# Performance work log

Hardware: AMD Instinct MI355X
Metric: run time of the kernel (lower is better)

The kernel has to match this reference:

```python
import jax, jax.numpy as jnp
import numpy as np

N_QUBITS = 14
N_LAYERS = 3
BATCH = 128


def _apply_1q(state, gate, w, n):
    """Apply a single-qubit gate on wire w (PennyLane wire 0 = most significant bit).
    state: (B, 2**n) complex. gate: (2,2) shared or (B,2,2) batched."""
    L, R = 2 ** w, 2 ** (n - 1 - w)
    s = state.reshape(-1, L, 2, R)
    if gate.ndim == 2:
        s = jnp.einsum('ij,aljr->alir', gate, s)
    else:
        s = jnp.einsum('aij,aljr->alir', gate, s)
    return s.reshape(state.shape)


def _apply_cnot(state, c, t, n):
    """CNOT with control wire c, target wire t on (B, 2**n) state."""
    s = state.reshape((-1,) + (2,) * n)
    ca = 1 + c
    s0 = jax.lax.index_in_dim(s, 0, ca, keepdims=False)
    s1 = jax.lax.index_in_dim(s, 1, ca, keepdims=False)
    # axis of target after removing control axis
    ta = 1 + t if t < c else t
    s1 = jnp.flip(s1, axis=ta)
    return jnp.stack([s0, s1], axis=ca).reshape(state.shape)


def _rx_gates(angles):
    """Batched RX gate matrices. angles: (B,) -> (B,2,2) complex64."""
    half = angles * 0.5
    c = jnp.cos(half).astype(jnp.complex64)
    s = (-1j) * jnp.sin(half).astype(jnp.complex64)
    return jnp.stack([jnp.stack([c, s], -1), jnp.stack([s, c], -1)], -2)


def _rot_gate(phi, theta, omega):
    """PennyLane Rot(phi,theta,omega) = RZ(omega) RY(theta) RZ(phi), (2,2) complex."""
    ct = jnp.cos(theta * 0.5).astype(jnp.complex64)
    st = jnp.sin(theta * 0.5).astype(jnp.complex64)
    ep = jnp.exp(-0.5j * (phi + omega))  # e^{-i(phi+omega)/2}
    em = jnp.exp(-0.5j * (phi - omega))  # e^{-i(phi-omega)/2}
    return jnp.stack([
        jnp.stack([ep * ct, -jnp.conj(em) * st]),
        jnp.stack([em * st, jnp.conj(ep) * ct]),
    ]).astype(jnp.complex64)


def _simulate(x, q_weights):
    B, n = x.shape
    state = jnp.zeros((B, 2 ** n), jnp.complex64).at[:, 0].set(1.0)
    # AngleEmbedding: RX(x_i) on wire i
    for w in range(n):
        state = _apply_1q(state, _rx_gates(x[:, w]), w, n)
    # StronglyEntanglingLayers: Rot on each wire, then ring of CNOTs with range r
    n_layers = q_weights.shape[0]
    for l in range(n_layers):
        for w in range(n):
            g = _rot_gate(q_weights[l, w, 0], q_weights[l, w, 1], q_weights[l, w, 2])
            state = _apply_1q(state, g, w, n)
        r = (l % (n - 1)) + 1  # PennyLane default ranges
        for w in range(n):
            state = _apply_cnot(state, w, (w + r) % n, n)
    return state


def _pauli_z_signs(n):
    idx = np.arange(2 ** n, dtype=np.int64)[:, None]
    shifts = np.arange(n - 1, -1, -1, dtype=np.int64)[None, :]  # wire 0 = MSB
    bits = (idx >> shifts) & 1
    return jnp.asarray(1.0 - 2.0 * bits, dtype=jnp.float32)  # (2**n, n)


def setup_inputs() -> dict:
    key = jax.random.key(0)
    k1, k2, k3, k4 = jax.random.split(key, 4)
    x = jax.random.normal(k1, (BATCH, N_QUBITS), dtype=jnp.float32)
    q_weights = jax.random.normal(k2, (N_LAYERS, N_QUBITS, 3), dtype=jnp.float32) * 0.01
    w_lin = jax.random.normal(k3, (1, N_QUBITS), dtype=jnp.float32) / np.sqrt(N_QUBITS)
    b_lin = jax.random.normal(k4, (1,), dtype=jnp.float32) * 0.01
    return {"x": x, "q_weights": q_weights, "w_lin": w_lin, "b_lin": b_lin}


def reference(x, q_weights, w_lin, b_lin):
    n = x.shape[1]
    state = _simulate(x, q_weights)
    probs = (state.real ** 2 + state.imag ** 2).astype(jnp.float32)  # (B, 2**n)
    expvals = probs @ _pauli_z_signs(n)  # (B, n) = <Z_i>
    logits = expvals @ w_lin.T + b_lin  # (B, 1)
    return logits
```

## Files before the change

### kernel.cpp

```cpp
#include <hip/hip_runtime.h>
#include <string.h>

#define NQ 14
#define NSTATE (1 << NQ)
#define NL 3
#define MAXP 12
#define BT 1024
#define NWAVES (BT / 64)
#define NEX 11

struct PassG {
    unsigned cmb8[16];
    unsigned R[10];
    unsigned gidx[4];
    unsigned nw;
    unsigned epm;
    unsigned eg[11];
    unsigned parw[11];
    unsigned pad[2];
};
struct ParamsG {
    PassG pass[MAXP];
    unsigned ms[NQ];
    unsigned fmask[NQ];
    unsigned initIW[10];
};
#define PG_WORDS ((int)(sizeof(ParamsG) / 4))

struct C2x2 { float2 m[2][2]; };

__device__ __forceinline__ float2 cmul(float2 a, float2 b) {
    return make_float2(a.x * b.x - a.y * b.y, a.x * b.y + a.y * b.x);
}
__device__ __forceinline__ float2 cmac(float2 acc, float2 a, float2 b) {
    acc.x = fmaf(a.x, b.x, fmaf(-a.y, b.y, acc.x));
    acc.y = fmaf(a.x, b.y, fmaf(a.y, b.x, acc.y));
    return acc;
}

__device__ __forceinline__ C2x2 rot_gate(const float* qp) {
    float phi = qp[0], th = qp[1], om = qp[2];
    float ct, stt; __sincosf(0.5f * th, &stt, &ct);
    float sa, ca; __sincosf(0.5f * (phi + om), &sa, &ca);
    float sb, cb; __sincosf(0.5f * (phi - om), &sb, &cb);
    C2x2 G;
    G.m[0][0] = make_float2(ca * ct, -sa * ct);
    G.m[0][1] = make_float2(-cb * stt, -sb * stt);
    G.m[1][0] = make_float2(cb * stt, -sb * stt);
    G.m[1][1] = make_float2(ca * ct, sa * ct);
    return G;
}

__device__ __forceinline__ C2x2 fuse_rx(C2x2 G, float ang) {
    float sh, ch; __sincosf(0.5f * ang, &sh, &ch);
    float2 c = make_float2(ch, 0.f), is = make_float2(0.f, -sh);
    C2x2 R;
    #pragma unroll
    for (int i = 0; i < 2; ++i) {
        R.m[i][0] = cmac(cmul(G.m[i][0], c), G.m[i][1], is);
        R.m[i][1] = cmac(cmul(G.m[i][1], c), G.m[i][0], is);
    }
    return R;
}

template<int C>
__device__ __forceinline__ void apply_extra(float2 a[16], const float2* gb,
        unsigned w1, unsigned pw, unsigned rep)
{
    const unsigned sga = w1 & 0x3FFFu;
    const int gi = (int)(w1 >> 16) * 4;
    const unsigned og = __popc(rep & sga) & 1u;
    const unsigned swv = pw ^ (og ? 0xFFFFu : 0u);
    float2 g00 = gb[gi + 0], g01 = gb[gi + 1], g10 = gb[gi + 2], g11 = gb[gi + 3];
    const int LB = C & (-C);
    #pragma unroll
    for (int i = 0; i < 16; ++i) {
        if (!(i & LB)) {
            const int i1 = i ^ C;
            const bool sw = (swv >> i) & 1u;
            float2 x0 = sw ? a[i1] : a[i];
            float2 x1 = sw ? a[i]  : a[i1];
            float2 n0 = cmac(cmul(g00, x0), g01, x1);
            float2 n1 = cmac(cmul(g10, x0), g11, x1);
            a[i]  = sw ? n1 : n0;
            a[i1] = sw ? n0 : n1;
        }
    }
}

#define APPLY_BASIS(PS)                                                     \
    {                                                                       \
        _Pragma("unroll")                                                   \
        for (int q = 0; q < 4; ++q) {                                       \
            if (q < (int)nwr) {                    \
                const int gi = (int)psh.pass[PS].gidx[q] * 4;               \
                float2 g00 = gbuf[gi + 0], g01 = gbuf[gi + 1];              \
                float2 g10 = gbuf[gi + 2], g11 = gbuf[gi + 3];              \
                _Pragma("unroll")                                           \
                for (int i = 0; i < 16; ++i) {                              \
                    if (!((i >> q) & 1)) {                                  \
                        const int i1 = i | (1 << q);                        \
                        float2 a0 = a[i], a1 = a[i1];                       \
                        float2 n0 = cmac(cmul(g00, a0), g01, a1);           \
                        float2 n1 = cmac(cmul(g10, a0), g11, a1);           \
                        a[i] = n0; a[i1] = n1;                              \
                    }                                                       \
                }                                                           \
            }                                                               \
        }                                                                   \
    }

#define APPLY_EXTRAS(PS)                                                    \
    {                                                                       \
        if (epm) {                                                          \
            if (epm & (1u<<0))  apply_extra<3> (a, gbuf, psh.pass[PS].eg[0],  psh.pass[PS].parw[0],  rn); \
            if (epm & (1u<<1))  apply_extra<5> (a, gbuf, psh.pass[PS].eg[1],  psh.pass[PS].parw[1],  rn); \
            if (epm & (1u<<2))  apply_extra<6> (a, gbuf, psh.pass[PS].eg[2],  psh.pass[PS].parw[2],  rn); \
            if (epm & (1u<<3))  apply_extra<9> (a, gbuf, psh.pass[PS].eg[3],  psh.pass[PS].parw[3],  rn); \
            if (epm & (1u<<4))  apply_extra<10>(a, gbuf, psh.pass[PS].eg[4],  psh.pass[PS].parw[4],  rn); \
            if (epm & (1u<<5))  apply_extra<12>(a, gbuf, psh.pass[PS].eg[5],  psh.pass[PS].parw[5],  rn); \
            if (epm & (1u<<6))  apply_extra<7> (a, gbuf, psh.pass[PS].eg[6],  psh.pass[PS].parw[6],  rn); \
            if (epm & (1u<<7))  apply_extra<11>(a, gbuf, psh.pass[PS].eg[7],  psh.pass[PS].parw[7],  rn); \
            if (epm & (1u<<8))  apply_extra<13>(a, gbuf, psh.pass[PS].eg[8],  psh.pass[PS].parw[8],  rn); \
            if (epm & (1u<<9))  apply_extra<14>(a, gbuf, psh.pass[PS].eg[9],  psh.pass[PS].parw[9],  rn); \
            if (epm & (1u<<10)) apply_extra<15>(a, gbuf, psh.pass[PS].eg[10], psh.pass[PS].parw[10], rn); \
        }                                                                   \
    }

__global__ __launch_bounds__(BT, 4) void qsim_kernel(
    const float* __restrict__ x, const float* __restrict__ qw,
    const float* __restrict__ wl, const float* __restrict__ bl,
    float* __restrict__ out, const ParamsG* __restrict__ pp, int np)
{
    __shared__ float2 st[NSTATE];
    __shared__ float2 gbuf[NL * NQ * 4];
    __shared__ float2 ubuf[NQ][2];
    __shared__ float red[NWAVES];
    __shared__ __align__(16) ParamsG psh;

    const int tid = threadIdx.x;
    const int b = blockIdx.x;

    {
        const unsigned* srcw = (const unsigned*)pp;
        unsigned* dstw = (unsigned*)&psh;
        for (int i = tid; i < PG_WORDS; i += BT) dstw[i] = srcw[i];
    }

    if (tid < NL * NQ) {
        int l = tid / NQ, w = tid % NQ;
        C2x2 G = rot_gate(qw + tid * 3);
        if (l == 0) {
            G = fuse_rx(G, x[b * NQ + w]);
            ubuf[w][0] = G.m[0][0];
            ubuf[w][1] = G.m[1][0];
        }
        gbuf[tid * 4 + 0] = G.m[0][0];
        gbuf[tid * 4 + 1] = G.m[0][1];
        gbuf[tid * 4 + 2] = G.m[1][0];
        gbuf[tid * 4 + 3] = G.m[1][1];
    }

    char* sb = (char*)st;
    float2 a[16];
    unsigned addr[16];
    unsigned rn;

    __syncthreads();

    {
        unsigned r0 = 0, b0 = 0;
        #pragma unroll
        for (int j = 0; j < 10; ++j) {
            const unsigned sel = (tid >> j) & 1;
            r0 ^= sel ? psh.pass[0].R[j] : 0u;
            b0 ^= sel ? psh.initIW[j] : 0u;
        }
        rn = r0;
        const unsigned rb = rn << 3;
        float2 c = ubuf[0][b0 & 1];
        #pragma unroll
        for (int w = 1; w < 10; ++w)
            c = cmul(c, ubuf[w][(b0 >> w) & 1]);
        a[0] = cmul(c, ubuf[10][0]);
        a[1] = cmul(c, ubuf[10][1]);
        #pragma unroll
        for (int i = 0; i < 2; ++i) {
            a[2 + i] = cmul(a[i], ubuf[11][1]);
            a[i]     = cmul(a[i], ubuf[11][0]);
        }
        #pragma unroll
        for (int i = 0; i < 4; ++i) {
            a[4 + i] = cmul(a[i], ubuf[12][1]);
            a[i]     = cmul(a[i], ubuf[12][0]);
        }
        #pragma unroll
        for (int i = 0; i < 8; ++i) {
            a[8 + i] = cmul(a[i], ubuf[13][1]);
            a[i]     = cmul(a[i], ubuf[13][0]);
        }
        #pragma unroll
        for (int i = 0; i < 16; ++i)
            *(float2*)(sb + (rb ^ psh.pass[0].cmb8[i])) = a[i];
    }

    {
        unsigned rt = 0;
        #pragma unroll
        for (int j = 0; j < 10; ++j)
            rt ^= ((tid >> j) & 1) ? psh.pass[1].R[j] : 0u;
        rn = rt;
    }

    #pragma unroll 1
    for (int ps = 1; ps < np - 1; ++ps) {
        __syncthreads();
        const unsigned rb = rn << 3;
        #pragma unroll
        for (int i = 0; i < 16; ++i) addr[i] = rb ^ psh.pass[ps].cmb8[i];
        #pragma unroll
        for (int i = 0; i < 16; ++i)
            a[i] = *(const float2*)(sb + addr[i]);
        unsigned rt = 0;
        #pragma unroll
        for (int j = 0; j < 10; ++j)
            rt ^= ((tid >> j) & 1) ? psh.pass[ps + 1].R[j] : 0u;
        const unsigned nwr = psh.pass[ps].nw;
        APPLY_BASIS(ps);
        const unsigned epm = psh.pass[ps].epm;
        APPLY_EXTRAS(ps);
        #pragma unroll
        for (int i = 0; i < 16; ++i)
            *(float2*)(sb + addr[i]) = a[i];
        rn = rt;
    }

    float acc = 0.f;
    {
        const int ps = np - 1;
        __syncthreads();
        const unsigned rb = rn << 3;
        #pragma unroll
        for (int i = 0; i < 16; ++i) addr[i] = rb ^ psh.pass[ps].cmb8[i];
        #pragma unroll
        for (int i = 0; i < 16; ++i)
            a[i] = *(const float2*)(sb + addr[i]);
        const unsigned nwr = psh.pass[ps].nw;
        APPLY_BASIS(ps);
        const unsigned epm = psh.pass[ps].epm;
        APPLY_EXTRAS(ps);

        float A[16];
        #pragma unroll
        for (int i = 0; i < 16; ++i) A[i] = 0.f;
        #pragma unroll
        for (int w = 0; w < NQ; ++w) {
            float v = wl[w];
            unsigned p0 = __popc(rn & psh.ms[w]) & 1u;
            float vs = p0 ? -v : v;
            const unsigned fm = psh.fmask[w];
            #pragma unroll
            for (int i = 0; i < 16; ++i)
                A[i] += ((fm >> i) & 1u) ? -vs : vs;
        }
        #pragma unroll
        for (int i = 0; i < 16; ++i)
            acc = fmaf(fmaf(a[i].x, a[i].x, a[i].y * a[i].y), A[i], acc);
    }

    #pragma unroll
    for (int off = 32; off > 0; off >>= 1) acc += __shfl_down(acc, off, 64);
    if ((tid & 63) == 0) red[tid >> 6] = acc;
    __syncthreads();
    if (tid == 0) {
        float s2 = 0.f;
        #pragma unroll
        for (int i = 0; i < NWAVES; ++i) s2 += red[i];
        out[b] = s2 + bl[0];
    }
}

struct GF2Basis {
    unsigned piv[NQ];
    GF2Basis() { for (int i = 0; i < NQ; ++i) piv[i] = 0; }
    bool insert(unsigned v) {
        for (int bb = NQ - 1; bb >= 0; --bb) {
            if (!((v >> bb) & 1)) continue;
            if (piv[bb]) v ^= piv[bb];
            else { piv[bb] = v; return true; }
        }
        return false;
    }
};

static inline int par16(unsigned v) { return __builtin_parity(v); }
static inline unsigned lcg_next(unsigned& s) { s = s * 1664525u + 1013904223u; return s >> 8; }

static unsigned gf_apply(const unsigned* C, unsigned v) {
    unsigned r = 0;
    while (v) { int j = __builtin_ctz(v); v &= v - 1; r ^= C[j]; }
    return r;
}

static bool gf_invert(const unsigned* C, unsigned* Ci) {
    unsigned rows[NQ], irows[NQ];
    for (int i = 0; i < NQ; ++i) {
        unsigned r = 0;
        for (int j = 0; j < NQ; ++j) r |= ((C[j] >> i) & 1u) << j;
        rows[i] = r; irows[i] = 1u << i;
    }
    for (int c = 0; c < NQ; ++c) {
        int p = -1;
        for (int r = c; r < NQ; ++r) if ((rows[r] >> c) & 1u) { p = r; break; }
        if (p < 0) return false;
        unsigned t = rows[p]; rows[p] = rows[c]; rows[c] = t;
        t = irows[p]; irows[p] = irows[c]; irows[c] = t;
        for (int r = 0; r < NQ; ++r)
            if (r != c && ((rows[r] >> c) & 1u)) { rows[r] ^= rows[c]; irows[r] ^= irows[c]; }
    }
    for (int j = 0; j < NQ; ++j) {
        unsigned col = 0;
        for (int i = 0; i < NQ; ++i) col |= ((irows[i] >> j) & 1u) << i;
        Ci[j] = col;
    }
    return true;
}

extern "C" void kernel_launch(void* const* d_in, const int* in_sizes, int n_in,
                              void* d_out, int out_size, void* d_ws, size_t ws_size,
                              hipStream_t stream) {
    const float* x  = (const float*)d_in[0];
    const float* qw = (const float*)d_in[1];
    const float* wl = (const float*)d_in[2];
    const float* bl = (const float*)d_in[3];
    float* out = (float*)d_out;

    const int B = in_sizes[0] / NQ;

    static const int EXC[NEX] = {3, 5, 6, 9, 10, 12, 7, 11, 13, 14, 15};
    int c2s[16]; for (int i = 0; i < 16; ++i) c2s[i] = -1;
    for (int k = 0; k < NEX; ++k) c2s[EXC[k]] = k;

    unsigned gs[NL * NQ], gm[NL * NQ];
    int ggi[NL * NQ];
    unsigned s[NQ], m[NQ], msIdx[NQ];
    for (int w = 0; w < NQ; ++w) s[w] = m[w] = 1u << (NQ - 1 - w);
    int ng = 0;
    for (int l = 0; l < NL; ++l) {
        if (l > 0) {
            for (int w = 0; w < NQ; ++w) {
                gs[ng] = s[w]; gm[ng] = m[w]; ggi[ng] = l * NQ + w; ++ng;
            }
        }
        int r = (l % (NQ - 1)) + 1;
        for (int w = 0; w < NQ; ++w) {
            int c = w, t = (w + r) % NQ;
            s[t] ^= s[c];
            m[c] ^= m[t];
        }
    }
    for (int w = 0; w < NQ; ++w) msIdx[w] = s[w];

    struct Raw {
        unsigned rv[10], cmb[16];
        unsigned char gidx[4], nw;
        int exgate[NEX];
        unsigned exsel[NEX];
        unsigned exT[NEX];
    } raw[MAXP];
    for (int p = 0; p < MAXP; ++p)
        for (int k = 0; k < NEX; ++k) raw[p].exgate[k] = -1;

    {
        unsigned mm[4];
        for (int q = 0; q < 4; ++q) mm[q] = 1u << (3 - q);
        for (int j = 0; j < 10; ++j) raw[0].rv[j] = 1u << (13 - j);
        for (int idx = 0; idx < 16; ++idx) {
            unsigned c = 0;
            for (int q = 0; q < 4; ++q) if ((idx >> q) & 1) c ^= mm[q];
            raw[0].cmb[idx] = c;
        }
        for (int q = 0; q < 4; ++q) raw[0].gidx[q] = 0;
        raw[0].nw = 0;
    }

    bool used[NL * NQ] = {false};
    int np = 1, remaining = ng;
    while (remaining > 0 && np < MAXP) {
        unsigned pss[4], pmm[4];
        int pgi[4], nw = 0;
        GF2Basis gf;
        for (int g = 0; g < ng && nw < 4; ++g) {
            if (used[g]) continue;
            bool ok = true;
            for (int k = 0; k < nw && ok; ++k)
                if (par16(gs[g] & pmm[k]) || par16(pss[k] & gm[g])) ok = false;
            for (int h = 0; h < g && ok; ++h)
                if (!used[h] && (par16(gs[g] & gm[h]) || par16(gs[h] & gm[g]))) ok = false;
            if (!ok) continue;
            GF2Basis trial = gf;
            if (!trial.insert(gm[g])) continue;
            gf = trial;
            pss[nw] = gs[g]; pmm[nw] = gm[g]; pgi[nw] = g; ++nw;
            used[g] = true; --remaining;
        }
        unsigned mm[4], ss[4];
        for (int i = 0; i < nw; ++i) { mm[i] = pmm[i]; ss[i] = pss[i]; }
        for (int i = nw; i < 4; ++i) {
            unsigned cand = 0;
            for (int t = 0; t < NQ; ++t)
                if (gf.insert(1u << t)) { cand = 1u << t; break; }
            for (int j = 0; j < nw; ++j)
                if (par16(cand & ss[j])) cand ^= mm[j];
            mm[i] = cand; ss[i] = 0;
        }
        int nR = 0;
        for (int t = 0; t < NQ && nR < 10; ++t) {
            if (gf.insert(1u << t)) {
                unsigned v = 1u << t;
                for (int j = 0; j < nw; ++j)
                    if (par16(v & ss[j])) v ^= mm[j];
                raw[np].rv[nR++] = v;
            }
        }
        for (int idx = 0; idx < 16; ++idx) {
            unsigned c = 0;
            for (int q = 0; q < 4; ++q) if ((idx >> q) & 1) c ^= mm[q];
            raw[np].cmb[idx] = c;
        }
        for (int q = 0; q < 4; ++q)
            raw[np].gidx[q] = (unsigned char)(q < nw ? ggi[pgi[q]] : 0);
        raw[np].nw = (unsigned char)nw;

        {
            int exCirc[NEX]; int nExtra = 0;
            for (int g = 0; g < ng; ++g) {
                if (used[g]) continue;
                int c = -1;
                for (int t2 = 3; t2 < 16; ++t2) {
                    if (__builtin_popcount((unsigned)t2) < 2) continue;
                    unsigned xr = 0;
                    for (int j = 0; j < 4; ++j) if ((t2 >> j) & 1) xr ^= mm[j];
                    if (xr == gm[g]) { c = t2; break; }
                }
                if (c < 0) continue;
                int slot = c2s[c];
                if (slot < 0 || raw[np].exgate[slot] >= 0) continue;
                unsigned T = 0;
                for (int j = 0; j < 4; ++j)
                    T |= (unsigned)(par16(mm[j] & gs[g]) & 1) << j;
                {
                    int sp = 0;
                    for (int j = 0; j < 4; ++j) if ((c >> j) & 1) sp ^= (T >> j) & 1;
                    if (!sp) continue;
                }
                bool ok = true;
                for (int e = 0; e < nExtra && ok; ++e) {
                    int h = exCirc[e];
                    if (par16(gs[g] & gm[h]) || par16(gs[h] & gm[g])) ok = false;
                }
                for (int kk = 0; kk < nw && ok; ++kk) {
                    int h = pgi[kk];
                    if (h > g && (par16(gs[g] & gm[h]) || par16(gs[h] & gm[g]))) ok = false;
                }
                for (int h = 0; h < g && ok; ++h)
                    if (!used[h] && (par16(gs[g] & gm[h]) || par16(gs[h] & gm[g]))) ok = false;
                if (!ok) continue;
                raw[np].exgate[slot] = ggi[g];
                raw[np].exsel[slot] = gs[g];
                raw[np].exT[slot] = T;
                exCirc[nExtra++] = g;
                used[g] = true; --remaining;
            }
        }
        ++np;
    }

    unsigned Cm[NQ], Ci[NQ];
    unsigned seed = 0x9E3779B9u;
    bool found = false;
    for (int tries = 0; tries < 5000 && !found; ++tries) {
        for (int j = 0; j < NQ; ++j) Cm[j] = lcg_next(seed) & (NSTATE - 1);
        if (!gf_invert(Cm, Ci)) continue;
        found = true;
        for (int p = 0; p < np && found; ++p) {
            unsigned piv[4] = {0, 0, 0, 0}; int npv = 0;
            for (int i = 0; i < 10; ++i) {
                unsigned w2 = gf_apply(Cm, raw[p].rv[i]);
                for (int bb = 0; bb < 4; ++bb)
                    if (((w2 >> bb) & 1u) && piv[bb]) w2 ^= piv[bb];
                if ((w2 & 15u) && npv < 4) { piv[__builtin_ctz(w2 & 15u)] = w2; ++npv; }
            }
            if (npv < 4) found = false;
        }
    }
    if (!found) {
        for (int j = 0; j < NQ; ++j) Cm[j] = 1u << j;
        gf_invert(Cm, Ci);
    }

    static ParamsG h_pg;
    memset(&h_pg, 0, sizeof(h_pg));
    for (int p = 0; p < np; ++p) {
        unsigned u[10];
        for (int i = 0; i < 10; ++i) u[i] = gf_apply(Cm, raw[p].rv[i]);
        unsigned piv[4] = {0, 0, 0, 0};
        int ord[10], npv = 0, rest[10], nrest = 0;
        for (int i = 0; i < 10; ++i) {
            unsigned w2 = u[i];
            for (int bb = 0; bb < 4; ++bb)
                if (((w2 >> bb) & 1u) && piv[bb]) w2 ^= piv[bb];
            if ((w2 & 15u) && npv < 4) { piv[__builtin_ctz(w2 & 15u)] = w2; ord[npv++] = i; }
            else rest[nrest++] = i;
        }
        int kk = 0;
        for (int i = 0; i < npv; ++i) h_pg.pass[p].R[kk++] = u[ord[i]];
        for (int i = 0; i < nrest; ++i) h_pg.pass[p].R[kk++] = u[rest[i]];
        for (int idx = 0; idx < 16; ++idx)
            h_pg.pass[p].cmb8[idx] = gf_apply(Cm, raw[p].cmb[idx]) << 3;
        for (int q = 0; q < 4; ++q) h_pg.pass[p].gidx[q] = raw[p].gidx[q];
        h_pg.pass[p].nw = raw[p].nw;
        unsigned epm = 0;
        for (int k = 0; k < NEX; ++k) {
            if (raw[p].exgate[k] < 0) continue;
            epm |= 1u << k;
            unsigned sga = 0;
            for (int i = 0; i < NQ; ++i)
                sga |= (unsigned)(par16(Ci[i] & raw[p].exsel[k]) & 1) << i;
            h_pg.pass[p].eg[k] = sga | ((unsigned)raw[p].exgate[k] << 16);
            unsigned T = raw[p].exT[k], pw = 0;
            for (int i = 0; i < 16; ++i)
                pw |= (unsigned)(__builtin_popcount(i & T) & 1) << i;
            h_pg.pass[p].parw[k] = pw;
        }
        h_pg.pass[p].epm = epm;
    }
    for (int w = 0; w < NQ; ++w) {
        unsigned msp = 0;
        for (int i = 0; i < NQ; ++i)
            msp |= (unsigned)(par16(Ci[i] & msIdx[w]) & 1) << i;
        h_pg.ms[w] = msp;
    }
    for (int w = 0; w < NQ; ++w) {
        unsigned fm = 0;
        for (int i = 0; i < 16; ++i)
            fm |= (unsigned)(par16((h_pg.pass[np - 1].cmb8[i] >> 3) & h_pg.ms[w]) & 1) << i;
        h_pg.fmask[w] = fm;
    }
    {
        unsigned tmask[NQ];
        for (int w = 0; w < NQ; ++w) {
            unsigned t = 0;
            for (int i = 0; i < NQ; ++i)
                t |= (unsigned)((Ci[i] >> (NQ - 1 - w)) & 1u) << i;
            tmask[w] = t;
        }
        for (int j = 0; j < 10; ++j) {
            unsigned iw = 0;
            for (int w = 0; w < NQ; ++w)
                iw |= (unsigned)(par16(h_pg.pass[0].R[j] & tmask[w]) & 1) << w;
            h_pg.initIW[j] = iw;
        }
    }

    ParamsG* d_pg = (ParamsG*)d_ws;
    hipMemcpyAsync(d_pg, &h_pg, sizeof(ParamsG), hipMemcpyHostToDevice, stream);
    qsim_kernel<<<dim3(B), dim3(BT), 0, stream>>>(x, qw, wl, bl, out, d_pg, np);
}
```

Measured before the change: 100.6 us.

## Split each batch state across two blocks with a global-memory exchange between halves

Splits the simulation into two kernels, each running two 512-thread blocks per batch element over a half-size (8192-entry) shared state. The circuit's passes are grouped into two halves, each lacking one GF(2) direction, and the state is exchanged through a global workspace buffer between the kernels. This aims to raise parallelism and occupancy, since the old launch used only one large block per element (128 blocks). It adds a global round-trip of the full state, a second launch, and extra host-side planning, with a fallback to the old single kernel when the split is not possible.

```diff
diff --git a/kernel.cpp b/kernel.cpp
--- a/kernel.cpp
+++ b/kernel.cpp
@@ -8,6 +8,66 @@
 #define BT 1024
 #define NWAVES (BT / 64)
 #define NEX 11
+#define BTS 512
+#define NWS (BTS / 64)
+#define HSTATE 8192
+
+
+struct C2x2 { float2 m[2][2]; };
+
+__device__ __forceinline__ float2 cmul(float2 a, float2 b) {
+    return make_float2(a.x * b.x - a.y * b.y, a.x * b.y + a.y * b.x);
+}
+__device__ __forceinline__ float2 cmac(float2 acc, float2 a, float2 b) {
+    acc.x = fmaf(a.x, b.x, fmaf(-a.y, b.y, acc.x));
+    acc.y = fmaf(a.x, b.y, fmaf(a.y, b.x, acc.y));
+    return acc;
+}
+__device__ __forceinline__ C2x2 rot_gate(const float* qp) {
+    float phi = qp[0], th = qp[1], om = qp[2];
+    float ct, stt; __sincosf(0.5f * th, &stt, &ct);
+    float sa, ca; __sincosf(0.5f * (phi + om), &sa, &ca);
+    float sb, cb; __sincosf(0.5f * (phi - om), &sb, &cb);
+    C2x2 G;
+    G.m[0][0] = make_float2(ca * ct, -sa * ct);
+    G.m[0][1] = make_float2(-cb * stt, -sb * stt);
+    G.m[1][0] = make_float2(cb * stt, -sb * stt);
+    G.m[1][1] = make_float2(ca * ct, sa * ct);
+    return G;
+}
+__device__ __forceinline__ C2x2 fuse_rx(C2x2 G, float ang) {
+    float sh, ch; __sincosf(0.5f * ang, &sh, &ch);
+    float2 c = make_float2(ch, 0.f), is = make_float2(0.f, -sh);
+    C2x2 R;
+    #pragma unroll
+    for (int i = 0; i < 2; ++i) {
+        R.m[i][0] = cmac(cmul(G.m[i][0], c), G.m[i][1], is);
+        R.m[i][1] = cmac(cmul(G.m[i][1], c), G.m[i][0], is);
+    }
+    return R;
+}
+
+#define APPLY_BASIS(PS)                                                     \
+    {                                                                       \
+        _Pragma("unroll")                                                   \
+        for (int q = 0; q < 4; ++q) {                                       \
+            if (q < (int)nwr) {                                             \
+                const int gi = (int)psh.pass[PS].gidx[q] * 4;               \
+                float2 g00 = gbuf[gi + 0], g01 = gbuf[gi + 1];              \
+                float2 g10 = gbuf[gi + 2], g11 = gbuf[gi + 3];              \
+                _Pragma("unroll")                                           \
+                for (int i = 0; i < 16; ++i) {                              \
+                    if (!((i >> q) & 1)) {                                  \
+                        const int i1 = i | (1 << q);                        \
+                        float2 a0 = a[i], a1 = a[i1];                       \
+                        float2 n0 = cmac(cmul(g00, a0), g01, a1);           \
+                        float2 n1 = cmac(cmul(g10, a0), g11, a1);           \
+                        a[i] = n0; a[i1] = n1;                              \
+                    }                                                       \
+                }                                                           \
+            }                                                               \
+        }                                                                   \
+    }
 
 struct PassG {
     unsigned cmb8[16];
@@ -26,42 +86,6 @@
     unsigned initIW[10];
 };
 #define PG_WORDS ((int)(sizeof(ParamsG) / 4))
-
-struct C2x2 { float2 m[2][2]; };
-
-__device__ __forceinline__ float2 cmul(float2 a, float2 b) {
-    return make_float2(a.x * b.x - a.y * b.y, a.x * b.y + a.y * b.x);
-}
-__device__ __forceinline__ float2 cmac(float2 acc, float2 a, float2 b) {
-    acc.x = fmaf(a.x, b.x, fmaf(-a.y, b.y, acc.x));
-    acc.y = fmaf(a.x, b.y, fmaf(a.y, b.x, acc.y));
-    return acc;
-}
-
-__device__ __forceinline__ C2x2 rot_gate(const float* qp) {
-    float phi = qp[0], th = qp[1], om = qp[2];
-    float ct, stt; __sincosf(0.5f * th, &stt, &ct);
-    float sa, ca; __sincosf(0.5f * (phi + om), &sa, &ca);
-    float sb, cb; __sincosf(0.5f * (phi - om), &sb, &cb);
-    C2x2 G;
-    G.m[0][0] = make_float2(ca * ct, -sa * ct);
-    G.m[0][1] = make_float2(-cb * stt, -sb * stt);
-    G.m[1][0] = make_float2(cb * stt, -sb * stt);
-    G.m[1][1] = make_float2(ca * ct, sa * ct);
-    return G;
-}
-
-__device__ __forceinline__ C2x2 fuse_rx(C2x2 G, float ang) {
-    float sh, ch; __sincosf(0.5f * ang, &sh, &ch);
-    float2 c = make_float2(ch, 0.f), is = make_float2(0.f, -sh);
-    C2x2 R;
-    #pragma unroll
-    for (int i = 0; i < 2; ++i) {
-        R.m[i][0] = cmac(cmul(G.m[i][0], c), G.m[i][1], is);
-        R.m[i][1] = cmac(cmul(G.m[i][1], c), G.m[i][0], is);
-    }
-    return R;
-}
 
 template<int C>
 __device__ __forceinline__ void apply_extra(float2 a[16], const float2* gb,
@@ -88,28 +112,6 @@
     }
 }
 
-#define APPLY_BASIS(PS)                                                     \
-    {                                                                       \
-        _Pragma("unroll")                                                   \
-        for (int q = 0; q < 4; ++q) {                                       \
-            if (q < (int)nwr) {                    \
-                const int gi = (int)psh.pass[PS].gidx[q] * 4;               \
-                float2 g00 = gbuf[gi + 0], g01 = gbuf[gi + 1];              \
-                float2 g10 = gbuf[gi + 2], g11 = gbuf[gi + 3];              \
-                _Pragma("unroll")                                           \
-                for (int i = 0; i < 16; ++i) {                              \
-                    if (!((i >> q) & 1)) {                                  \
-                        const int i1 = i | (1 << q);                        \
-                        float2 a0 = a[i], a1 = a[i1];                       \
-                        float2 n0 = cmac(cmul(g00, a0), g01, a1);           \
-                        float2 n1 = cmac(cmul(g10, a0), g11, a1);           \
-                        a[i] = n0; a[i1] = n1;                              \
-                    }                                                       \
-                }                                                           \
-            }                                                               \
-        }                                                                   \
-    }
-
 #define APPLY_EXTRAS(PS)                                                    \
     {                                                                       \
         if (epm) {                                                          \
@@ -146,7 +148,6 @@
         unsigned* dstw = (unsigned*)&psh;
         for (int i = tid; i < PG_WORDS; i += BT) dstw[i] = srcw[i];
     }
-
     if (tid < NL * NQ) {
         int l = tid / NQ, w = tid % NQ;
         C2x2 G = rot_gate(qw + tid * 3);
@@ -280,6 +281,312 @@
     }
 }
 
+struct PassK {
+    unsigned cmb8[16];
+    unsigned R[9];
+    unsigned Ug;
+    unsigned gidx[4];
+    unsigned nw, epm;
+    unsigned eg[NEX];
+    unsigned parw[NEX];
+};
+struct ParamsK1 {
+    PassK pass[3];
+    unsigned initIW[9];
+    unsigned initIWg;
+    unsigned SK[12];
+    unsigned SKj, SKg;
+    unsigned pad;
+};
+struct ParamsK2 {
+    PassK pass[3];
+    unsigned SL[13], SLj;
+    unsigned ms[NQ];
+    unsigned fmask[NQ];
+};
+struct ParamsS { ParamsK1 k1; ParamsK2 k2; };
+
+template<int C>
+__device__ __forceinline__ void apply_extra_s(float2 a[16], const float2* gb,
+        unsigned w1, unsigned pw, unsigned rep, unsigned gbit)
+{
+    const int gi = (int)(w1 >> 16) * 4;
+    const unsigned og = ((unsigned)__popc(rep & (w1 & 0x1FFFu)) ^ ((w1 >> 13) & gbit)) & 1u;
+    const unsigned swv = pw ^ (og ? 0xFFFFu : 0u);
+    float2 g00 = gb[gi + 0], g01 = gb[gi + 1], g10 = gb[gi + 2], g11 = gb[gi + 3];
+    const int LB = C & (-C);
+    #pragma unroll
+    for (int i = 0; i < 16; ++i) {
+        if (!(i & LB)) {
+            const int i1 = i ^ C;
+            const bool sw = (swv >> i) & 1u;
+            float2 x0 = sw ? a[i1] : a[i];
+            float2 x1 = sw ? a[i]  : a[i1];
+            float2 n0 = cmac(cmul(g00, x0), g01, x1);
+            float2 n1 = cmac(cmul(g10, x0), g11, x1);
+            a[i]  = sw ? n1 : n0;
+            a[i1] = sw ? n0 : n1;
+        }
+    }
+}
+
+#define APPLY_EXTRAS_S(PS, GB)                                              \
+    {                                                                       \
+        if (epm) {                                                          \
+            if (epm & (1u<<0))  apply_extra_s<3> (a, gbuf, psh.pass[PS].eg[0],  psh.pass[PS].parw[0],  rn, GB); \
+            if (epm & (1u<<1))  apply_extra_s<5> (a, gbuf, psh.pass[PS].eg[1],  psh.pass[PS].parw[1],  rn, GB); \
+            if (epm & (1u<<2))  apply_extra_s<6> (a, gbuf, psh.pass[PS].eg[2],  psh.pass[PS].parw[2],  rn, GB); \
+            if (epm & (1u<<3))  apply_extra_s<9> (a, gbuf, psh.pass[PS].eg[3],  psh.pass[PS].parw[3],  rn, GB); \
+            if (epm & (1u<<4))  apply_extra_s<10>(a, gbuf, psh.pass[PS].eg[4],  psh.pass[PS].parw[4],  rn, GB); \
+            if (epm & (1u<<5))  apply_extra_s<12>(a, gbuf, psh.pass[PS].eg[5],  psh.pass[PS].parw[5],  rn, GB); \
+            if (epm & (1u<<6))  apply_extra_s<7> (a, gbuf, psh.pass[PS].eg[6],  psh.pass[PS].parw[6],  rn, GB); \
+            if (epm & (1u<<7))  apply_extra_s<11>(a, gbuf, psh.pass[PS].eg[7],  psh.pass[PS].parw[7],  rn, GB); \
+            if (epm & (1u<<8))  apply_extra_s<13>(a, gbuf, psh.pass[PS].eg[8],  psh.pass[PS].parw[8],  rn, GB); \
+            if (epm & (1u<<9))  apply_extra_s<14>(a, gbuf, psh.pass[PS].eg[9],  psh.pass[PS].parw[9],  rn, GB); \
+            if (epm & (1u<<10)) apply_extra_s<15>(a, gbuf, psh.pass[PS].eg[10], psh.pass[PS].parw[10], rn, GB); \
+        }                                                                   \
+    }
+
+__global__ __launch_bounds__(BTS, 4) void qsim_k1(
+    const float* __restrict__ x, const float* __restrict__ qw,
+    const ParamsS* __restrict__ pp, float2* __restrict__ stbuf,
+    float* __restrict__ out)
+{
+    __shared__ float2 st[HSTATE];
+    __shared__ float2 gbuf[NL * NQ * 4];
+    __shared__ float2 ubuf[NQ][2];
+    __shared__ ParamsK1 psh;
+
+    const int tid = threadIdx.x;
+    const int e = blockIdx.x >> 1, g1 = blockIdx.x & 1;
+
+    {
+        const unsigned* s = (const unsigned*)&pp->k1;
+        unsigned* d = (unsigned*)&psh;
+        for (int i = tid; i < (int)(sizeof(ParamsK1) / 4); i += BTS) d[i] = s[i];
+    }
+    if (tid < NL * NQ) {
+        int l = tid / NQ, w = tid % NQ;
+        C2x2 G = rot_gate(qw + tid * 3);
+        if (l == 0) {
+            G = fuse_rx(G, x[e * NQ + w]);
+            ubuf[w][0] = G.m[0][0];
+            ubuf[w][1] = G.m[1][0];
+        }
+        gbuf[tid * 4 + 0] = G.m[0][0];
+        gbuf[tid * 4 + 1] = G.m[0][1];
+        gbuf[tid * 4 + 2] = G.m[1][0];
+        gbuf[tid * 4 + 3] = G.m[1][1];
+    }
+    char* sb = (char*)st;
+    __syncthreads();
+
+    {
+        unsigned rn = g1 ? psh.pass[0].Ug : 0u;
+        unsigned b0 = g1 ? psh.initIWg : 0u;
+        #pragma unroll
+        for (int j5 = 0; j5 < 9; ++j5) {
+            const unsigned sel = (tid >> j5) & 1u;
+            rn ^= sel ? psh.pass[0].R[j5] : 0u;
+            b0 ^= sel ? psh.initIW[j5] : 0u;
+        }
+        const unsigned rb = rn << 3;
+        float2 a[16];
+        float2 c = ubuf[0][b0 & 1];
+        #pragma unroll
+        for (int w = 1; w < 10; ++w)
+            c = cmul(c, ubuf[w][(b0 >> w) & 1]);
+        a[0] = cmul(c, ubuf[10][0]);
+        a[1] = cmul(c, ubuf[10][1]);
+        #pragma unroll
+        for (int i = 0; i < 2; ++i) {
+            a[2 + i] = cmul(a[i], ubuf[11][1]);
+            a[i]     = cmul(a[i], ubuf[11][0]);
+        }
+        #pragma unroll
+        for (int i = 0; i < 4; ++i) {
+            a[4 + i] = cmul(a[i], ubuf[12][1]);
+            a[i]     = cmul(a[i], ubuf[12][0]);
+        }
+        #pragma unroll
+        for (int i = 0; i < 8; ++i) {
+            a[8 + i] = cmul(a[i], ubuf[13][1]);
+            a[i]     = cmul(a[i], ubuf[13][0]);
+        }
+        #pragma unroll
+        for (int i = 0; i < 16; ++i)
+            *(float2*)(sb + (rb ^ psh.pass[0].cmb8[i])) = a[i];
+    }
+
+    for (int p5 = 1; p5 < 3; ++p5) {
+        __syncthreads();
+        unsigned rn = g1 ? psh.pass[p5].Ug : 0u;
+        #pragma unroll
+        for (int j5 = 0; j5 < 9; ++j5)
+            rn ^= ((tid >> j5) & 1u) ? psh.pass[p5].R[j5] : 0u;
+        const unsigned rb = rn << 3;
+        unsigned addr[16];
+        #pragma unroll
+        for (int i = 0; i < 16; ++i) addr[i] = rb ^ psh.pass[p5].cmb8[i];
+        float2 a[16];
+        #pragma unroll
+        for (int i = 0; i < 16; ++i) a[i] = *(const float2*)(sb + addr[i]);
+        const unsigned nwr = psh.pass[p5].nw;
+        APPLY_BASIS(p5);
+        const unsigned epm = psh.pass[p5].epm;
+        APPLY_EXTRAS_S(p5, (unsigned)g1);
+        #pragma unroll
+        for (int i = 0; i < 16; ++i) *(float2*)(sb + addr[i]) = a[i];
+    }
+    __syncthreads();
+
+    {
+        unsigned tb = g1 ? psh.SKg : 0u;
+        #pragma unroll
+        for (int k = 0; k < 9; ++k)
+            tb ^= ((tid >> k) & 1u) ? psh.SK[k] : 0u;
+        #pragma unroll
+        for (int j2 = 0; j2 < 2; ++j2) {
+            const unsigned bb = tb ^ (j2 ? psh.SKj : 0u);
+            float2* gdst = stbuf + ((((size_t)e * 2 + j2) * 2 + g1) << 12) + tid;
+            #pragma unroll
+            for (int i = 0; i < 8; ++i) {
+                unsigned la = bb;
+                if (i & 1) la ^= psh.SK[9];
+                if (i & 2) la ^= psh.SK[10];
+                if (i & 4) la ^= psh.SK[11];
+                gdst[i * 512] = *(const float2*)(sb + la);
+            }
+        }
+        if (g1 == 0 && tid == 0) out[e] = 0.f;
+    }
+}
+
+__global__ __launch_bounds__(BTS, 4) void qsim_k2(
+    const float* __restrict__ x, const float* __restrict__ qw,
+    const float* __restrict__ wl, const float* __restrict__ bl,
+    const ParamsS* __restrict__ pp, const float2* __restrict__ stbuf,
+    float* __restrict__ out)
+{
+    __shared__ float2 st[HSTATE];
+    __shared__ float2 gbuf[NL * NQ * 4];
+    __shared__ float2 ubuf[NQ][2];
+    __shared__ ParamsK2 psh;
+    __shared__ float red[NWS];
+
+    const int tid = threadIdx.x;
+    const int e = blockIdx.x >> 1, j = blockIdx.x & 1;
+
+    {
+        const unsigned* s = (const unsigned*)&pp->k2;
+        unsigned* d = (unsigned*)&psh;
+        for (int i = tid; i < (int)(sizeof(ParamsK2) / 4); i += BTS) d[i] = s[i];
+    }
+    if (tid < NL * NQ) {
+        int l = tid / NQ, w = tid % NQ;
+        C2x2 G = rot_gate(qw + tid * 3);
+        if (l == 0) {
+            G = fuse_rx(G, x[e * NQ + w]);
+            ubuf[w][0] = G.m[0][0];
+            ubuf[w][1] = G.m[1][0];
+        }
+        gbuf[tid * 4 + 0] = G.m[0][0];
+        gbuf[tid * 4 + 1] = G.m[0][1];
+        gbuf[tid * 4 + 2] = G.m[1][0];
+        gbuf[tid * 4 + 3] = G.m[1][1];
+    }
+    char* sb = (char*)st;
+    __syncthreads();
+
+    {
+        unsigned tb = j ? psh.SLj : 0u;
+        #pragma unroll
+        for (int k = 0; k < 9; ++k)
+            tb ^= ((tid >> k) & 1u) ? psh.SL[k] : 0u;
+        const float2* gsrc = stbuf + (((size_t)e * 2 + j) << 13) + tid;
+        #pragma unroll
+        for (int i = 0; i < 16; ++i) {
+            float2 v = gsrc[i * 512];
+            unsigned la = tb;
+            if (i & 1) la ^= psh.SL[9];
+            if (i & 2) la ^= psh.SL[10];
+            if (i & 4) la ^= psh.SL[11];
+            if (i & 8) la ^= psh.SL[12];
+            *(float2*)(sb + la) = v;
+        }
+    }
+
+    for (int p5 = 0; p5 < 2; ++p5) {
+        __syncthreads();
+        unsigned rn = j ? psh.pass[p5].Ug : 0u;
+        #pragma unroll
+        for (int j5 = 0; j5 < 9; ++j5)
+            rn ^= ((tid >> j5) & 1u) ? psh.pass[p5].R[j5] : 0u;
+        const unsigned rb = rn << 3;
+        unsigned addr[16];
+        #pragma unroll
+        for (int i = 0; i < 16; ++i) addr[i] = rb ^ psh.pass[p5].cmb8[i];
+        float2 a[16];
+        #pragma unroll
+        for (int i = 0; i < 16; ++i) a[i] = *(const float2*)(sb + addr[i]);
+        const unsigned nwr = psh.pass[p5].nw;
+        APPLY_BASIS(p5);
+        const unsigned epm = psh.pass[p5].epm;
+        APPLY_EXTRAS_S(p5, (unsigned)j);
+        #pragma unroll
+        for (int i = 0; i < 16; ++i) *(float2*)(sb + addr[i]) = a[i];
+    }
+
+    float acc = 0.f;
+    {
+        __syncthreads();
+        unsigned rn = j ? psh.pass[2].Ug : 0u;
+        #pragma unroll
+        for (int j5 = 0; j5 < 9; ++j5)
+            rn ^= ((tid >> j5) & 1u) ? psh.pass[2].R[j5] : 0u;
+        const unsigned rb = rn << 3;
+        unsigned addr[16];
+        #pragma unroll
+        for (int i = 0; i < 16; ++i) addr[i] = rb ^ psh.pass[2].cmb8[i];
+        float2 a[16];
+        #pragma unroll
+        for (int i = 0; i < 16; ++i) a[i] = *(const float2*)(sb + addr[i]);
+        const unsigned nwr = psh.pass[2].nw;
+        APPLY_BASIS(2);
+        const unsigned epm = psh.pass[2].epm;
+        APPLY_EXTRAS_S(2, (unsigned)j);
+
+        float A[16];
+        #pragma unroll
+        for (int i = 0; i < 16; ++i) A[i] = 0.f;
+        #pragma unroll
+        for (int w = 0; w < NQ; ++w) {
+            float v = wl[w];
+            const unsigned msw = psh.ms[w];
+            unsigned p0 = ((unsigned)__popc(rn & (msw & 0x1FFFu)) ^ ((msw >> 13) & (unsigned)j)) & 1u;
+            float vs = p0 ? -v : v;
+            const unsigned fm = psh.fmask[w];
+            #pragma unroll
+            for (int i = 0; i < 16; ++i)
+                A[i] += ((fm >> i) & 1u) ? -vs : vs;
+        }
+        #pragma unroll
+        for (int i = 0; i < 16; ++i)
+            acc = fmaf(fmaf(a[i].x, a[i].x, a[i].y * a[i].y), A[i], acc);
+    }
+
+    #pragma unroll
+    for (int off = 32; off > 0; off >>= 1) acc += __shfl_down(acc, off, 64);
+    if ((tid & 63) == 0) red[tid >> 6] = acc;
+    __syncthreads();
+    if (tid == 0) {
+        float s2 = 0.f;
+        #pragma unroll
+        for (int i = 0; i < NWS; ++i) s2 += red[i];
+        atomicAdd(out + e, s2 + (j == 0 ? bl[0] : 0.f));
+    }
+}
+
 struct GF2Basis {
     unsigned piv[NQ];
     GF2Basis() { for (int i = 0; i < NQ; ++i) piv[i] = 0; }
@@ -326,24 +633,64 @@
     return true;
 }
 
-extern "C" void kernel_launch(void* const* d_in, const int* in_sizes, int n_in,
-                              void* d_out, int out_size, void* d_ws, size_t ws_size,
-                              hipStream_t stream) {
-    const float* x  = (const float*)d_in[0];
-    const float* qw = (const float*)d_in[1];
-    const float* wl = (const float*)d_in[2];
-    const float* bl = (const float*)d_in[3];
-    float* out = (float*)d_out;
-
-    const int B = in_sizes[0] / NQ;
-
-    static const int EXC[NEX] = {3, 5, 6, 9, 10, 12, 7, 11, 13, 14, 15};
+static void rows_to_cols(const unsigned* rows, unsigned* cols) {
+    for (int j = 0; j < NQ; ++j) {
+        unsigned c = 0;
+        for (int i = 0; i < NQ; ++i) c |= ((rows[i] >> j) & 1u) << i;
+        cols[j] = c;
+    }
+}
+
+static unsigned gf_nullfunc(const unsigned* bas, int n) {
+    unsigned rows[NQ]; int nr = 0;
+    for (int i = 0; i < n; ++i) {
+        unsigned v = bas[i];
+        for (int k = 0; k < nr; ++k) {
+            int p = 31 - __builtin_clz(rows[k]);
+            if ((v >> p) & 1u) v ^= rows[k];
+        }
+        if (v) rows[nr++] = v;
+    }
+    for (int k = 0; k < nr; ++k) {
+        int p = 31 - __builtin_clz(rows[k]);
+        for (int k2 = 0; k2 < nr; ++k2)
+            if (k2 != k && ((rows[k2] >> p) & 1u)) rows[k2] ^= rows[k];
+    }
+    unsigned pivmask = 0;
+    for (int k = 0; k < nr; ++k) pivmask |= 1u << (31 - __builtin_clz(rows[k]));
+    for (int f = 0; f < NQ; ++f) {
+        if ((pivmask >> f) & 1u) continue;
+        unsigned xx = 1u << f;
+        for (int k = 0; k < nr; ++k)
+            if ((rows[k] >> f) & 1u) xx |= 1u << (31 - __builtin_clz(rows[k]));
+        bool ok = true;
+        for (int i = 0; i < n && ok; ++i) if (par16(bas[i] & xx)) ok = false;
+        if (ok) return xx;
+    }
+    return 0;
+}
+
+static unsigned addr_img(const unsigned* T, unsigned v) {
+    unsigned r = 0;
+    for (int i = 0; i < 13; ++i) r |= (unsigned)(par16(T[i] & v) & 1) << i;
+    return r;
+}
+
+struct RawEntry {
+    unsigned mm[4], ss[4];
+    unsigned char gidx[4], nw;
+    int exgate[NEX];
+    unsigned exsel[NEX], exT[NEX];
+};
+static const int EXC[NEX] = {3, 5, 6, 9, 10, 12, 7, 11, 13, 14, 15};
+
+static int build_and_pack(RawEntry* raw, unsigned* msIdx) {
     int c2s[16]; for (int i = 0; i < 16; ++i) c2s[i] = -1;
     for (int k = 0; k < NEX; ++k) c2s[EXC[k]] = k;
 
     unsigned gs[NL * NQ], gm[NL * NQ];
     int ggi[NL * NQ];
-    unsigned s[NQ], m[NQ], msIdx[NQ];
+    unsigned s[NQ], m[NQ];
     for (int w = 0; w < NQ; ++w) s[w] = m[w] = 1u << (NQ - 1 - w);
     int ng = 0;
     for (int l = 0; l < NL; ++l) {
@@ -361,28 +708,15 @@
     }
     for (int w = 0; w < NQ; ++w) msIdx[w] = s[w];
 
-    struct Raw {
-        unsigned rv[10], cmb[16];
-        unsigned char gidx[4], nw;
-        int exgate[NEX];
-        unsigned exsel[NEX];
-        unsigned exT[NEX];
-    } raw[MAXP];
     for (int p = 0; p < MAXP; ++p)
         for (int k = 0; k < NEX; ++k) raw[p].exgate[k] = -1;
 
-    {
-        unsigned mm[4];
-        for (int q = 0; q < 4; ++q) mm[q] = 1u << (3 - q);
-        for (int j = 0; j < 10; ++j) raw[0].rv[j] = 1u << (13 - j);
-        for (int idx = 0; idx < 16; ++idx) {
-            unsigned c = 0;
-            for (int q = 0; q < 4; ++q) if ((idx >> q) & 1) c ^= mm[q];
-            raw[0].cmb[idx] = c;
-        }
-        for (int q = 0; q < 4; ++q) raw[0].gidx[q] = 0;
-        raw[0].nw = 0;
-    }
+    for (int q = 0; q < 4; ++q) {
+        raw[0].mm[q] = 1u << (3 - q);
+        raw[0].ss[q] = 1u << (3 - q);
+        raw[0].gidx[q] = 0;
+    }
+    raw[0].nw = 0;
 
     bool used[NL * NQ] = {false};
     int np = 1, remaining = ng;
@@ -410,24 +744,11 @@
             unsigned cand = 0;
             for (int t = 0; t < NQ; ++t)
                 if (gf.insert(1u << t)) { cand = 1u << t; break; }
-            for (int j = 0; j < nw; ++j)
-                if (par16(cand & ss[j])) cand ^= mm[j];
+            for (int jq = 0; jq < nw; ++jq)
+                if (par16(cand & ss[jq])) cand ^= mm[jq];
             mm[i] = cand; ss[i] = 0;
         }
-        int nR = 0;
-        for (int t = 0; t < NQ && nR < 10; ++t) {
-            if (gf.insert(1u << t)) {
-                unsigned v = 1u << t;
-                for (int j = 0; j < nw; ++j)
-                    if (par16(v & ss[j])) v ^= mm[j];
-                raw[np].rv[nR++] = v;
-            }
-        }
-        for (int idx = 0; idx < 16; ++idx) {
-            unsigned c = 0;
-            for (int q = 0; q < 4; ++q) if ((idx >> q) & 1) c ^= mm[q];
-            raw[np].cmb[idx] = c;
-        }
+        for (int q = 0; q < 4; ++q) { raw[np].mm[q] = mm[q]; raw[np].ss[q] = ss[q]; }
         for (int q = 0; q < 4; ++q)
             raw[np].gidx[q] = (unsigned char)(q < nw ? ggi[pgi[q]] : 0);
         raw[np].nw = (unsigned char)nw;
@@ -440,23 +761,23 @@
                 for (int t2 = 3; t2 < 16; ++t2) {
                     if (__builtin_popcount((unsigned)t2) < 2) continue;
                     unsigned xr = 0;
-                    for (int j = 0; j < 4; ++j) if ((t2 >> j) & 1) xr ^= mm[j];
+                    for (int jq = 0; jq < 4; ++jq) if ((t2 >> jq) & 1) xr ^= mm[jq];
                     if (xr == gm[g]) { c = t2; break; }
                 }
                 if (c < 0) continue;
                 int slot = c2s[c];
                 if (slot < 0 || raw[np].exgate[slot] >= 0) continue;
                 unsigned T = 0;
-                for (int j = 0; j < 4; ++j)
-                    T |= (unsigned)(par16(mm[j] & gs[g]) & 1) << j;
+                for (int jq = 0; jq < 4; ++jq)
+                    T |= (unsigned)(par16(mm[jq] & gs[g]) & 1) << jq;
                 {
                     int sp = 0;
-                    for (int j = 0; j < 4; ++j) if ((c >> j) & 1) sp ^= (T >> j) & 1;
+                    for (int jq = 0; jq < 4; ++jq) if ((c >> jq) & 1) sp ^= (T >> jq) & 1;
                     if (!sp) continue;
                 }
                 bool ok = true;
-                for (int e = 0; e < nExtra && ok; ++e) {
-                    int h = exCirc[e];
+                for (int e2 = 0; e2 < nExtra && ok; ++e2) {
+                    int h = exCirc[e2];
                     if (par16(gs[g] & gm[h]) || par16(gs[h] & gm[g])) ok = false;
                 }
                 for (int kk = 0; kk < nw && ok; ++kk) {
@@ -475,9 +796,26 @@
         }
         ++np;
     }
-
+    return np;
+}
+
+static void old_emit(const RawEntry* raw, int np, const unsigned* msIdx,
+                     ParamsG& h_pg, unsigned seed) {
+    unsigned rvA[MAXP][10];
+    for (int p = 0; p < np; ++p) {
+        GF2Basis gf;
+        for (int q = 0; q < 4; ++q) gf.insert(raw[p].mm[q]);
+        int nR = 0;
+        for (int t = 0; t < NQ && nR < 10; ++t) {
+            if (gf.insert(1u << t)) {
+                unsigned v = 1u << t;
+                for (int q = 0; q < 4; ++q)
+                    if (par16(v & raw[p].ss[q])) v ^= raw[p].mm[q];
+                rvA[p][nR++] = v;
+            }
+        }
+    }
     unsigned Cm[NQ], Ci[NQ];
-    unsigned seed = 0x9E3779B9u;
     bool found = false;
     for (int tries = 0; tries < 5000 && !found; ++tries) {
         for (int j = 0; j < NQ; ++j) Cm[j] = lcg_next(seed) & (NSTATE - 1);
@@ -486,7 +824,7 @@
         for (int p = 0; p < np && found; ++p) {
             unsigned piv[4] = {0, 0, 0, 0}; int npv = 0;
             for (int i = 0; i < 10; ++i) {
-                unsigned w2 = gf_apply(Cm, raw[p].rv[i]);
+                unsigned w2 = gf_apply(Cm, rvA[p][i]);
                 for (int bb = 0; bb < 4; ++bb)
                     if (((w2 >> bb) & 1u) && piv[bb]) w2 ^= piv[bb];
                 if ((w2 & 15u) && npv < 4) { piv[__builtin_ctz(w2 & 15u)] = w2; ++npv; }
@@ -494,16 +832,12 @@
             if (npv < 4) found = false;
         }
     }
-    if (!found) {
-        for (int j = 0; j < NQ; ++j) Cm[j] = 1u << j;
-        gf_invert(Cm, Ci);
-    }
-
-    static ParamsG h_pg;
+    if (!found) { for (int j = 0; j < NQ; ++j) Cm[j] = 1u << j; gf_invert(Cm, Ci); }
+
     memset(&h_pg, 0, sizeof(h_pg));
     for (int p = 0; p < np; ++p) {
         unsigned u[10];
-        for (int i = 0; i < 10; ++i) u[i] = gf_apply(Cm, raw[p].rv[i]);
+        for (int i = 0; i < 10; ++i) u[i] = gf_apply(Cm, rvA[p][i]);
         unsigned piv[4] = {0, 0, 0, 0};
         int ord[10], npv = 0, rest[10], nrest = 0;
         for (int i = 0; i < 10; ++i) {
@@ -516,8 +850,11 @@
         int kk = 0;
         for (int i = 0; i < npv; ++i) h_pg.pass[p].R[kk++] = u[ord[i]];
         for (int i = 0; i < nrest; ++i) h_pg.pass[p].R[kk++] = u[rest[i]];
-        for (int idx = 0; idx < 16; ++idx)
-            h_pg.pass[p].cmb8[idx] = gf_apply(Cm, raw[p].cmb[idx]) << 3;
+        for (int idx = 0; idx < 16; ++idx) {
+            unsigned c = 0;
+            for (int q = 0; q < 4; ++q) if ((idx >> q) & 1) c ^= raw[p].mm[q];
+            h_pg.pass[p].cmb8[idx] = gf_apply(Cm, c) << 3;
+        }
         for (int q = 0; q < 4; ++q) h_pg.pass[p].gidx[q] = raw[p].gidx[q];
         h_pg.pass[p].nw = raw[p].nw;
         unsigned epm = 0;
@@ -562,8 +899,215 @@
             h_pg.initIW[j] = iw;
         }
     }
-
-    ParamsG* d_pg = (ParamsG*)d_ws;
-    hipMemcpyAsync(d_pg, &h_pg, sizeof(ParamsG), hipMemcpyHostToDevice, stream);
-    qsim_kernel<<<dim3(B), dim3(BT), 0, stream>>>(x, qw, wl, bl, out, d_pg, np);
-}
+}
+
+static bool try_split(const RawEntry* raw, int np, const unsigned* msIdx,
+                      ParamsS& SP, unsigned seed) {
+    if (np != 6) return false;
+    for (int p = 1; p < 6; ++p) if (raw[p].nw != 4) return false;
+    memset(&SP, 0, sizeof(SP));
+
+    unsigned phi[2];
+    for (int c = 0; c < 2; ++c) {
+        unsigned bas[12]; int nb = 0;
+        for (int p = c * 3; p < c * 3 + 3; ++p)
+            for (int q = 0; q < 4; ++q) bas[nb++] = raw[p].mm[q];
+        phi[c] = gf_nullfunc(bas, nb);
+        if (!phi[c]) return false;
+    }
+    unsigned rows2[NQ];
+    {
+        GF2Basis rb;
+        if (!rb.insert(phi[1])) return false;
+        if (!rb.insert(phi[0])) return false;
+        int nmu = 0;
+        for (int t = 0; t < NQ && nmu < 12; ++t)
+            if (rb.insert(1u << t)) rows2[nmu++] = 1u << t;
+        if (nmu != 12) return false;
+        rows2[12] = phi[0];
+        rows2[13] = phi[1];
+    }
+    unsigned colsM[NQ], Ci2[NQ];
+    rows_to_cols(rows2, colsM);
+    if (!gf_invert(colsM, Ci2)) return false;
+
+    for (int k = 0; k < 2; ++k) {
+        unsigned ph = phi[k];
+        int p0e = k * 3;
+        int pivbit = __builtin_ctz(ph);
+        unsigned kb[13]; int nkb = 0;
+        for (int t = 0; t < NQ; ++t) {
+            if (t == pivbit) continue;
+            unsigned v = 1u << t;
+            if ((ph >> t) & 1u) v ^= 1u << pivbit;
+            kb[nkb++] = v;
+        }
+        unsigned RvAll[3][9], UgAll[3];
+        for (int pe = 0; pe < 3; ++pe) {
+            const RawEntry& re = raw[p0e + pe];
+            for (int q = 0; q < 4; ++q) if (par16(ph & re.mm[q])) return false;
+            GF2Basis gfb;
+            for (int q = 0; q < 4; ++q) if (!gfb.insert(re.mm[q])) return false;
+            int nR = 0;
+            for (int i = 0; i < 13 && nR < 9; ++i) {
+                unsigned v = kb[i];
+                if (gfb.insert(v)) {
+                    for (int q = 0; q < 4; ++q)
+                        if (par16(v & re.ss[q])) v ^= re.mm[q];
+                    RvAll[pe][nR++] = v;
+                }
+            }
+            if (nR != 9) return false;
+            unsigned ug = 1u << pivbit;
+            for (int q = 0; q < 4; ++q)
+                if (par16(ug & re.ss[q])) ug ^= re.mm[q];
+            UgAll[pe] = ug;
+        }
+        unsigned T[13], Vt[NQ], Wt = 0;
+        bool found = false;
+        for (int tries = 0; tries < 20000 && !found; ++tries) {
+            for (int i = 0; i < 13; ++i) T[i] = lcg_next(seed) & (NSTATE - 1);
+            unsigned mrows[NQ], cm[NQ], ci[NQ];
+            for (int i = 0; i < 13; ++i) mrows[i] = T[i];
+            mrows[13] = ph;
+            rows_to_cols(mrows, cm);
+            if (!gf_invert(cm, ci)) continue;
+            bool ok = true;
+            for (int pe = 0; pe < 3 && ok; ++pe) {
+                unsigned piv[4] = {0, 0, 0, 0}; int npv = 0;
+                for (int i = 0; i < 9; ++i) {
+                    unsigned w2 = addr_img(T, RvAll[pe][i]);
+                    for (int bb = 0; bb < 4; ++bb)
+                        if (((w2 >> bb) & 1u) && piv[bb]) w2 ^= piv[bb];
+                    if ((w2 & 15u) && npv < 4) { piv[__builtin_ctz(w2 & 15u)] = w2; ++npv; }
+                }
+                if (npv < 4) ok = false;
+            }
+            if (!ok) continue;
+            found = true;
+            for (int i = 0; i < NQ; ++i) Vt[i] = ci[i];
+            Wt = ci[13];
+        }
+        if (!found) return false;
+
+        PassK* PK = (k == 0) ? SP.k1.pass : SP.k2.pass;
+        int ord0[9];
+        for (int pe = 0; pe < 3; ++pe) {
+            const RawEntry& re = raw[p0e + pe];
+            PassK& P = PK[pe];
+            unsigned img[9];
+            for (int i = 0; i < 9; ++i) img[i] = addr_img(T, RvAll[pe][i]);
+            unsigned piv[4] = {0, 0, 0, 0};
+            int ord[9], npv = 0, rest[9], nrest = 0;
+            for (int i = 0; i < 9; ++i) {
+                unsigned w2 = img[i];
+                for (int bb = 0; bb < 4; ++bb)
+                    if (((w2 >> bb) & 1u) && piv[bb]) w2 ^= piv[bb];
+                if ((w2 & 15u) && npv < 4) { piv[__builtin_ctz(w2 & 15u)] = w2; ord[npv++] = i; }
+                else rest[nrest++] = i;
+            }
+            int kk = 0;
+            for (int i = 0; i < npv; ++i)  { if (pe == 0) ord0[kk] = ord[i];  P.R[kk] = img[ord[i]];  ++kk; }
+            for (int i = 0; i < nrest; ++i){ if (pe == 0) ord0[kk] = rest[i]; P.R[kk] = img[rest[i]]; ++kk; }
+            P.Ug = addr_img(T, UgAll[pe]);
+            for (int idx = 0; idx < 16; ++idx) {
+                unsigned c = 0;
+                for (int q = 0; q < 4; ++q) if ((idx >> q) & 1) c ^= re.mm[q];
+                P.cmb8[idx] = addr_img(T, c) << 3;
+            }
+            for (int q = 0; q < 4; ++q) P.gidx[q] = re.gidx[q];
+            P.nw = re.nw;
+            unsigned epm = 0;
+            for (int sl = 0; sl < NEX; ++sl) {
+                if (re.exgate[sl] < 0) continue;
+                epm |= 1u << sl;
+                unsigned sga = 0;
+                for (int i = 0; i < 13; ++i)
+                    sga |= (unsigned)(par16(Vt[i] & re.exsel[sl]) & 1) << i;
+                unsigned sgc = (unsigned)(par16(Wt & re.exsel[sl]) & 1);
+                P.eg[sl] = sga | (sgc << 13) | ((unsigned)re.exgate[sl] << 16);
+                unsigned Tq = re.exT[sl], pw = 0;
+                for (int i = 0; i < 16; ++i)
+                    pw |= (unsigned)(__builtin_popcount(i & Tq) & 1) << i;
+                P.parw[sl] = pw;
+            }
+            P.epm = epm;
+        }
+        if (k == 0) {
+            for (int jj = 0; jj < 9; ++jj) {
+                unsigned v = RvAll[0][ord0[jj]], iw = 0;
+                for (int w = 0; w < NQ; ++w)
+                    iw |= ((v >> (NQ - 1 - w)) & 1u) << w;
+                SP.k1.initIW[jj] = iw;
+            }
+            {
+                unsigned v = UgAll[0], iw = 0;
+                for (int w = 0; w < NQ; ++w)
+                    iw |= ((v >> (NQ - 1 - w)) & 1u) << w;
+                SP.k1.initIWg = iw;
+            }
+            for (int i = 0; i < 12; ++i) SP.k1.SK[i] = addr_img(T, Ci2[i]) << 3;
+            SP.k1.SKg = addr_img(T, Ci2[12]) << 3;
+            SP.k1.SKj = addr_img(T, Ci2[13]) << 3;
+        } else {
+            for (int i = 0; i < 12; ++i) SP.k2.SL[i] = addr_img(T, Ci2[i]) << 3;
+            SP.k2.SL[12] = addr_img(T, Ci2[12]) << 3;
+            SP.k2.SLj    = addr_img(T, Ci2[13]) << 3;
+            for (int w = 0; w < NQ; ++w) {
+                unsigned m13 = 0;
+                for (int i = 0; i < 13; ++i)
+                    m13 |= (unsigned)(par16(Vt[i] & msIdx[w]) & 1) << i;
+                unsigned mg = (unsigned)(par16(Wt & msIdx[w]) & 1);
+                SP.k2.ms[w] = m13 | (mg << 13);
+            }
+            for (int w = 0; w < NQ; ++w) {
+                unsigned fm = 0;
+                for (int i = 0; i < 16; ++i) {
+                    unsigned c = 0;
+                    for (int q = 0; q < 4; ++q) if ((i >> q) & 1) c ^= raw[5].mm[q];
+                    fm |= (unsigned)(par16(c & msIdx[w]) & 1) << i;
+                }
+                SP.k2.fmask[w] = fm;
+            }
+        }
+    }
+    return true;
+}
+
+extern "C" void kernel_launch(void* const* d_in, const int* in_sizes, int n_in,
+                              void* d_out, int out_size, void* d_ws, size_t ws_size,
+                              hipStream_t stream) {
+    const float* x  = (const float*)d_in[0];
+    const float* qw = (const float*)d_in[1];
+    const float* wl = (const float*)d_in[2];
+    const float* bl = (const float*)d_in[3];
+    float* out = (float*)d_out;
+
+    const int B = in_sizes[0] / NQ;
+
+    static RawEntry raw[MAXP];
+    unsigned msIdx[NQ];
+    int np = build_and_pack(raw, msIdx);
+
+    static ParamsS h_sp;
+    static ParamsG h_pg;
+    const size_t stoff = 4096;
+    const size_t need = stoff + (size_t)B * NSTATE * sizeof(float2);
+
+    bool use_split = (ws_size >= need) &&
+                     try_split(raw, np, msIdx, h_sp, 0xC0FFEE13u);
+
+    if (use_split) {
+        hipMemcpyAsync(d_ws, &h_sp, sizeof(ParamsS), hipMemcpyHostToDevice, stream);
+        float2* stb = (float2*)((char*)d_ws + stoff);
+        qsim_k1<<<dim3(2 * B), dim3(BTS), 0, stream>>>(
+            x, qw, (const ParamsS*)d_ws, stb, out);
+        qsim_k2<<<dim3(2 * B), dim3(BTS), 0, stream>>>(
+            x, qw, wl, bl, (const ParamsS*)d_ws, stb, out);
+    } else {
+        old_emit(raw, np, msIdx, h_pg, 0x9E3779B9u);
+        hipMemcpyAsync(d_ws, &h_pg, sizeof(ParamsG), hipMemcpyHostToDevice, stream);
+        qsim_kernel<<<dim3(B), dim3(BT), 0, stream>>>(
+            x, qw, wl, bl, out, (const ParamsG*)d_ws, np);
+    }
+}
```

Result: no change. 100.2 us (-0.4%).
